# Optimization experiments

Measured on AMD Instinct MI355X. Metric: run time of the kernel, lower is better.

## Reference

```python
import jax, jax.numpy as jnp
import numpy as np

B, LQ, LKV, H, D, HS = 8, 32, 4096, 16, 64, 1024
ROPE_THETA = 10000.0
MAX_POS = 2080


def setup_inputs() -> dict:
    key = jax.random.key(0)
    ks = jax.random.split(key, 7)
    scale = 0.02
    return {
        "hidden_states": jax.random.normal(ks[0], (B, LQ, HS), dtype=jnp.float32),
        "encoder_hidden_states": jax.random.normal(ks[1], (B, LKV, HS), dtype=jnp.float32),
        "position_ids_q": jax.random.randint(ks[2], (B, LQ), 0, MAX_POS, dtype=jnp.int64),
        "Wq": jax.random.normal(ks[3], (HS, HS), dtype=jnp.float32) * scale,
        "Wk": jax.random.normal(ks[4], (HS, HS), dtype=jnp.float32) * scale,
        "Wv": jax.random.normal(ks[5], (HS, HS), dtype=jnp.float32) * scale,
        "Wo": jax.random.normal(ks[6], (HS, HS), dtype=jnp.float32) * scale,
    }


def _rotate_half(x):
    x1, x2 = jnp.split(x, 2, axis=-1)
    return jnp.concatenate([-x2, x1], axis=-1)


def _rope_cos_sin(position_ids):
    # LLaMA-style rotary embedding: inv_freq over even dims, emb = [freqs, freqs]
    inv_freq = 1.0 / (ROPE_THETA ** (jnp.arange(0, D, 2, dtype=jnp.float32) / D))
    freqs = position_ids.astype(jnp.float32)[..., None] * inv_freq  # [B, LQ, D/2]
    emb = jnp.concatenate([freqs, freqs], axis=-1)                  # [B, LQ, D]
    # broadcast over heads: [B, 1, LQ, D]
    return jnp.cos(emb)[:, None], jnp.sin(emb)[:, None]


def reference(hidden_states, encoder_hidden_states, position_ids_q, Wq, Wk, Wv, Wo):
    bsz, q_len, _ = hidden_states.shape
    kv_len = encoder_hidden_states.shape[1]
    # projections (weights stored [in, out])
    q = hidden_states @ Wq                       # [B, LQ, HS]
    k = encoder_hidden_states @ Wk               # [B, LKV, HS]
    v = encoder_hidden_states @ Wv               # [B, LKV, HS]
    # split heads -> [B, H, L, D]
    q = q.reshape(bsz, q_len, H, D).transpose(0, 2, 1, 3)
    k = k.reshape(bsz, kv_len, H, D).transpose(0, 2, 1, 3)
    v = v.reshape(bsz, kv_len, H, D).transpose(0, 2, 1, 3)
    # RoPE applied to QUERY ONLY (per original module)
    cos, sin = _rope_cos_sin(position_ids_q)
    q = q * cos + _rotate_half(q) * sin
    # scaled dot-product cross attention
    scores = jnp.einsum("bhqd,bhkd->bhqk", q, k) / jnp.sqrt(jnp.asarray(D, q.dtype))
    attn = jax.nn.softmax(scores, axis=-1)
    out = jnp.einsum("bhqk,bhkd->bhqd", attn, v)  # [B, H, LQ, D]
    out = out.transpose(0, 2, 1, 3).reshape(bsz, q_len, HS)
    return out @ Wo
```

## Files before the change

### kernel.cpp

```cpp
#include <hip/hip_runtime.h>


typedef float  f32x4  __attribute__((ext_vector_type(4)));
typedef __bf16 bf16x8 __attribute__((ext_vector_type(8)));

__device__ __forceinline__ ushort f2b(float x) {
  union { float f; unsigned u; } v; v.f = x;
  unsigned r = (v.u + 0x7fffu + ((v.u >> 16) & 1u)) >> 16;
  return (ushort)r;
}
__device__ __forceinline__ float b2f(ushort h) {
  union { unsigned u; float f; } v; v.u = ((unsigned)h) << 16; return v.f;
}
__device__ __forceinline__ void unpack2(unsigned v, float& lo, float& hi) {
  union { unsigned u; float f; } a, b;
  a.u = v << 16; b.u = v & 0xffff0000u;
  lo = a.f; hi = b.f;
}
__device__ __forceinline__ unsigned packb(float a, float b) {
  return (unsigned)f2b(a) | ((unsigned)f2b(b) << 16);
}
__device__ __forceinline__ int swz(int r) { return (r & 3) ^ ((r >> 2) & 3); }

__device__ __forceinline__ void gload16(const void* g, void* l) {
  __builtin_amdgcn_global_load_lds(
      (const __attribute__((address_space(1))) void*)g,
      (__attribute__((address_space(3))) void*)l, 16, 0, 0);
}

__global__ __launch_bounds__(256) void pack_x(
    const float* __restrict__ X, ushort* __restrict__ Xp1, ushort* __restrict__ Xp2) {
  const int z = blockIdx.z, jb = blockIdx.y, cb = blockIdx.x;
  const int t = threadIdx.x;
  __shared__ ushort sT[128 * 72];

#pragma unroll
  for (int rep = 0; rep < 2; ++rep) {
    const int j  = rep * 64 + (t >> 2);
    const int c0 = (t & 3) << 4;
    const float4* src = (const float4*)(X + ((size_t)z * 4096 + jb * 128 + j) * 1024 + cb * 64 + c0);
#pragma unroll
    for (int q = 0; q < 4; ++q) {
      const float4 v = src[q];
      ushort4 w; w.x = f2b(v.x); w.y = f2b(v.y); w.z = f2b(v.z); w.w = f2b(v.w);
      *(ushort4*)&sT[j * 72 + c0 + q * 4] = w;
    }
  }
  __syncthreads();

  ushort* o1 = Xp1 + ((size_t)(z * 32 + jb) * 32 + cb * 2) * 4096;
#pragma unroll
  for (int q = 0; q < 4; ++q) {
    const int kih = q >> 1;
    const int r   = ((q & 1) << 6) + (t >> 2);
    const int p   = t & 3;
    const int lc  = p ^ swz(r);
    const uint4 v = *(const uint4*)&sT[r * 72 + kih * 32 + lc * 8];
    *(uint4*)&o1[(size_t)kih * 4096 + ((size_t)(q & 1) << 11) + (size_t)t * 8] = v;
  }

  ushort* o2 = Xp2 + (((size_t)(z * 8 + (cb >> 1)) * 128 + jb * 4) * 4096) + ((size_t)(cb & 1) << 11);
#pragma unroll
  for (int q = 0; q < 4; ++q) {
    const int cl = t >> 2;
    const int p2 = t & 3;
    const int lj = p2 ^ swz(cl);
    union { ushort u[8]; uint4 v; } pk;
#pragma unroll
    for (int jj = 0; jj < 8; ++jj) pk.u[jj] = sT[(q * 32 + lj * 8 + jj) * 72 + cl];
    *(uint4*)&o2[(size_t)q * 4096 + (size_t)t * 8] = pk.v;
  }
}

__global__ __launch_bounds__(256) void pack_w(
    const float* __restrict__ Wq, const float* __restrict__ Wk,
    const float* __restrict__ Wv, const float* __restrict__ Wo,
    ushort* __restrict__ WqT, ushort* __restrict__ Wkb,
    ushort* __restrict__ WvT, ushort* __restrict__ WoT) {
  const int wsel = blockIdx.z;
  const float* src = (wsel == 0) ? Wq : (wsel == 1) ? Wk : (wsel == 2) ? Wv : Wo;
  const int row0 = blockIdx.y << 6, col0 = blockIdx.x << 6;
  const int t = threadIdx.x;
  __shared__ ushort sT[64 * 72];
  const int r = t >> 2, c0 = (t & 3) << 4;

  union { ushort u[16]; uint4 v[2]; } pk;
  const float4* s4 = (const float4*)(src + (size_t)(row0 + r) * 1024 + col0 + c0);
#pragma unroll
  for (int q = 0; q < 4; ++q) {
    const float4 v = s4[q];
    pk.u[q*4+0] = f2b(v.x); pk.u[q*4+1] = f2b(v.y);
    pk.u[q*4+2] = f2b(v.z); pk.u[q*4+3] = f2b(v.w);
  }
  if (wsel == 1) {
    ushort* dst = Wkb + (size_t)(row0 + r) * 1024 + col0 + c0;
    *(uint4*)dst = pk.v[0];
    *(uint4*)(dst + 8) = pk.v[1];
  } else {
#pragma unroll
    for (int q = 0; q < 16; ++q) sT[r * 72 + c0 + q] = pk.u[q];
    __syncthreads();
    ushort* dst = (wsel == 0) ? WqT : (wsel == 2) ? WvT : WoT;
    union { ushort u[16]; uint4 v[2]; } o;
#pragma unroll
    for (int q = 0; q < 16; ++q) o.u[q] = sT[(c0 + q) * 72 + r];
    ushort* d = dst + (size_t)(col0 + r) * 1024 + row0 + c0;
    *(uint4*)d = o.v[0];
    *(uint4*)(d + 8) = o.v[1];
  }
}

__global__ __launch_bounds__(256) void qrope_gemm(
    const float* __restrict__ hs, const ushort* __restrict__ WqT,
    float* __restrict__ qP) {
  __shared__ alignas(16) ushort sA[128 * 40];
  __shared__ alignas(16) ushort sB[128 * 40];
  const int nt = blockIdx.x, mt = blockIdx.y, ks = blockIdx.z;
  const int m0 = mt << 7, n0 = nt << 7, kb = ks << 8;
  const int t = threadIdx.x;
  const int wave = t >> 6, lane = t & 63;
  const int wm = wave >> 1, wn = wave & 1;
  const int fr = lane & 15, fq = lane >> 4;
  const int r = t >> 1, sg = (t & 1) << 4;

  f32x4 acc[4][4];
#pragma unroll
  for (int a = 0; a < 4; ++a)
#pragma unroll
    for (int c = 0; c < 4; ++c) acc[a][c] = (f32x4){0.f, 0.f, 0.f, 0.f};

  for (int it = 0; it < 8; ++it) {
    const int k0 = kb + (it << 5);
    {
      const float4* s4 = (const float4*)(hs + (size_t)(m0 + r) * 1024 + k0 + sg);
      union { ushort u[16]; uint4 v[2]; } pk;
#pragma unroll
      for (int q = 0; q < 4; ++q) {
        const float4 v = s4[q];
        pk.u[q*4+0] = f2b(v.x); pk.u[q*4+1] = f2b(v.y);
        pk.u[q*4+2] = f2b(v.z); pk.u[q*4+3] = f2b(v.w);
      }
      *(uint4*)&sA[r * 40 + sg]     = pk.v[0];
      *(uint4*)&sA[r * 40 + sg + 8] = pk.v[1];
    }
    {
      const uint4* s4 = (const uint4*)(WqT + (size_t)(n0 + r) * 1024 + k0 + sg);
      *(uint4*)&sB[r * 40 + sg]     = s4[0];
      *(uint4*)&sB[r * 40 + sg + 8] = s4[1];
    }
    __syncthreads();
    bf16x8 aF[4], bF[4];
#pragma unroll
    for (int u = 0; u < 4; ++u) {
      aF[u] = *(const bf16x8*)&sA[((wm << 6) + (u << 4) + fr) * 40 + (fq << 3)];
      bF[u] = *(const bf16x8*)&sB[((wn << 6) + (u << 4) + fr) * 40 + (fq << 3)];
    }
#pragma unroll
    for (int mi = 0; mi < 4; ++mi)
#pragma unroll
      for (int ni = 0; ni < 4; ++ni)
        acc[mi][ni] = __builtin_amdgcn_mfma_f32_16x16x32_bf16(
            aF[mi], bF[ni], acc[mi][ni], 0, 0, 0);
    __syncthreads();
  }
  float* dst = qP + (size_t)ks * 262144;
#pragma unroll
  for (int mi = 0; mi < 4; ++mi)
#pragma unroll
    for (int ni = 0; ni < 4; ++ni)
#pragma unroll
      for (int rr = 0; rr < 4; ++rr) {
        const int row = m0 + (wm << 6) + (mi << 4) + (fq << 2) + rr;
        const int col = n0 + (wn << 6) + (ni << 4) + fr;
        dst[(size_t)row * 1024 + col] = acc[mi][ni][rr];
      }
}

__global__ __launch_bounds__(256) void rope_apply(
    const float* __restrict__ qP, const int* __restrict__ pos,
    ushort* __restrict__ qr) {
  const int idx = blockIdx.x * 256 + threadIdx.x;
  const int m = idx >> 6;
  const int u = idx & 63;
  const int h = u >> 2;
  const int c8 = (u & 3) << 3;
  const int colx = h * 64 + c8;
  const int coly = colx + 32;

  float x[8], y[8];
#pragma unroll
  for (int j = 0; j < 8; ++j) { x[j] = 0.f; y[j] = 0.f; }
#pragma unroll
  for (int p = 0; p < 4; ++p) {
    const float* base = qP + (size_t)p * 262144 + (size_t)m * 1024;
    const float4 a0 = *(const float4*)(base + colx);
    const float4 a1 = *(const float4*)(base + colx + 4);
    const float4 b0 = *(const float4*)(base + coly);
    const float4 b1 = *(const float4*)(base + coly + 4);
    x[0]+=a0.x; x[1]+=a0.y; x[2]+=a0.z; x[3]+=a0.w;
    x[4]+=a1.x; x[5]+=a1.y; x[6]+=a1.z; x[7]+=a1.w;
    y[0]+=b0.x; y[1]+=b0.y; y[2]+=b0.z; y[3]+=b0.w;
    y[4]+=b1.x; y[5]+=b1.y; y[6]+=b1.z; y[7]+=b1.w;
  }

  unsigned oddor = 0;
  for (int j = 1; j < 256; j += 2) oddor |= (unsigned)pos[j];
  const int p = (oddor == 0) ? pos[2 * m] : pos[m];
  const float pf = (float)p;

  union { ushort u16[8]; uint4 v; } ox, oy;
#pragma unroll
  for (int j = 0; j < 8; ++j) {
    const int f = c8 + j;
    const float inv = powf(10000.0f, -(float)f * (1.0f / 32.0f));
    float sn, cs; sincosf(pf * inv, &sn, &cs);
    ox.u16[j] = f2b((x[j] * cs - y[j] * sn) * 0.125f);
    oy.u16[j] = f2b((y[j] * cs + x[j] * sn) * 0.125f);
  }
  *(uint4*)(qr + (size_t)m * 1024 + colx) = ox.v;
  *(uint4*)(qr + (size_t)m * 1024 + coly) = oy.v;
}

__global__ __launch_bounds__(256) void qk_gemm(
    const ushort* __restrict__ qr, const ushort* __restrict__ Wkb,
    ushort* __restrict__ qk) {
  __shared__ alignas(16) ushort sA[32 * 72];
  __shared__ alignas(16) ushort sB[256 * 72];
  const int nc = blockIdx.x, h = blockIdx.y, b = blockIdx.z;
  const int t = threadIdx.x;
  {
    const int i = t >> 3, seg = (t & 7) << 3;
    *(uint4*)&sA[i * 72 + seg] =
        *(const uint4*)(qr + (size_t)(b * 32 + i) * 1024 + h * 64 + seg);
  }
#pragma unroll
  for (int p = 0; p < 8; ++p) {
    const int rr = (t >> 3) + p * 32, seg = (t & 7) << 3;
    *(uint4*)&sB[rr * 72 + seg] =
        *(const uint4*)(Wkb + (size_t)(nc * 256 + rr) * 1024 + h * 64 + seg);
  }
  __syncthreads();

  const int wave = t >> 6, lane = t & 63;
  const int fr = lane & 15, fq = lane >> 4;
  f32x4 acc[2][4];
#pragma unroll
  for (int a = 0; a < 2; ++a)
#pragma unroll
    for (int c = 0; c < 4; ++c) acc[a][c] = (f32x4){0.f, 0.f, 0.f, 0.f};

#pragma unroll
  for (int ki = 0; ki < 2; ++ki) {
    bf16x8 aF[2], bF[4];
#pragma unroll
    for (int mi = 0; mi < 2; ++mi)
      aF[mi] = *(const bf16x8*)&sA[((mi << 4) + fr) * 72 + (ki << 5) + (fq << 3)];
#pragma unroll
    for (int ni = 0; ni < 4; ++ni)
      bF[ni] = *(const bf16x8*)&sB[((wave << 6) + (ni << 4) + fr) * 72 + (ki << 5) + (fq << 3)];
#pragma unroll
    for (int mi = 0; mi < 2; ++mi)
#pragma unroll
      for (int ni = 0; ni < 4; ++ni)
        acc[mi][ni] = __builtin_amdgcn_mfma_f32_16x16x32_bf16(
            aF[mi], bF[ni], acc[mi][ni], 0, 0, 0);
  }
#pragma unroll
  for (int mi = 0; mi < 2; ++mi)
#pragma unroll
    for (int ni = 0; ni < 4; ++ni)
#pragma unroll
      for (int rr = 0; rr < 4; ++rr) {
        const int row = h * 32 + (mi << 4) + (fq << 2) + rr;
        const int col = nc * 256 + (wave << 6) + (ni << 4) + fr;
        qk[((size_t)b * 512 + row) * 1024 + col] = f2b(acc[mi][ni][rr]);
      }
}

__global__ __launch_bounds__(256) void gemm1(
    const ushort* __restrict__ qk, const ushort* __restrict__ Xp1,
    ushort* __restrict__ Sc, float2* __restrict__ pstat) {
  __shared__ alignas(16) ushort sA[4096];
  __shared__ alignas(16) ushort sB[4096];
  __shared__ float sMx[256], sSm[256];
  const int z = blockIdx.x, nty = blockIdx.y, mt = blockIdx.z;
  const int tid = threadIdx.x;
  const int wave = tid >> 6, lane = tid & 63;
  const int wm = wave >> 1, wn = wave & 1;
  const int fr = lane & 15, fq = lane >> 4;
  const int sfr = swz(fr);
  const int srow = lane >> 2;
  const int lc   = (lane & 3) ^ swz(srow);

  const ushort* Ab = qk + ((size_t)z * 512 + mt * 128) * 1024;
  const ushort* Bb = Xp1 + ((size_t)(z * 32 + nty) * 32) * 4096;

  f32x4 acc[4][4];
#pragma unroll
  for (int a = 0; a < 4; ++a)
#pragma unroll
    for (int c = 0; c < 4; ++c) acc[a][c] = (f32x4){0.f, 0.f, 0.f, 0.f};

  for (int it = 0; it < 32; ++it) {
    const int k0 = it << 5;
    const ushort* Bc = Bb + (size_t)it * 4096 + wave * 1024;
#pragma unroll
    for (int seg = 0; seg < 2; ++seg) {
      gload16(Bc + seg * 512 + lane * 8, &sB[wave * 1024 + seg * 512]);
      const int row = wave * 32 + seg * 16 + srow;
      gload16(Ab + (size_t)row * 1024 + k0 + lc * 8, &sA[wave * 1024 + seg * 512]);
    }
    __syncthreads();
    bf16x8 aF[4], bF[4];
#pragma unroll
    for (int u = 0; u < 4; ++u) {
      aF[u] = *(const bf16x8*)&sA[((wm << 6) + (u << 4) + fr) * 32 + ((fq ^ sfr) << 3)];
      bF[u] = *(const bf16x8*)&sB[((wn << 6) + (u << 4) + fr) * 32 + ((fq ^ sfr) << 3)];
    }
#pragma unroll
    for (int mi = 0; mi < 4; ++mi)
#pragma unroll
      for (int nt = 0; nt < 4; ++nt)
        acc[mi][nt] = __builtin_amdgcn_mfma_f32_16x16x32_bf16(
            aF[mi], bF[nt], acc[mi][nt], 0, 0, 0);
    __syncthreads();
  }

  ushort* ScB = Sc + (size_t)(z * 4 + mt) * 524288;
#pragma unroll
  for (int mi = 0; mi < 4; ++mi)
#pragma unroll
    for (int nt = 0; nt < 4; ++nt)
#pragma unroll
      for (int r = 0; r < 4; ++r) {
        const int row = (wm << 6) + (mi << 4) + (fq << 2) + r;
        const int col = (wn << 6) + (nt << 4) + fr;
        const int ki  = (nty << 2) + (col >> 5);
        const int p   = ((col >> 3) & 3) ^ r ^ fq;
        const ushort hb = f2b(acc[mi][nt][r]);
        ScB[(size_t)ki * 4096 + row * 32 + p * 8 + (fr & 7)] = hb;
        acc[mi][nt][r] = b2f(hb);
      }

#pragma unroll
  for (int mi = 0; mi < 4; ++mi)
#pragma unroll
    for (int r = 0; r < 4; ++r) {
      float m4 = fmaxf(fmaxf(acc[mi][0][r], acc[mi][1][r]),
                       fmaxf(acc[mi][2][r], acc[mi][3][r]));
#pragma unroll
      for (int o = 1; o < 16; o <<= 1) m4 = fmaxf(m4, __shfl_xor(m4, o));
      float s4 = __expf(acc[mi][0][r] - m4) + __expf(acc[mi][1][r] - m4) +
                 __expf(acc[mi][2][r] - m4) + __expf(acc[mi][3][r] - m4);
#pragma unroll
      for (int o = 1; o < 16; o <<= 1) s4 += __shfl_xor(s4, o);
      if (fr == 0) {
        const int row = (wm << 6) + (mi << 4) + (fq << 2) + r;
        sMx[row * 2 + wn] = m4;
        sSm[row * 2 + wn] = s4;
      }
    }
  __syncthreads();
  if (tid < 128) {
    const float m0 = sMx[tid * 2], m1 = sMx[tid * 2 + 1];
    const float M = fmaxf(m0, m1);
    const float S = sSm[tid * 2] * __expf(m0 - M) + sSm[tid * 2 + 1] * __expf(m1 - M);
    pstat[((size_t)(z * 512 + mt * 128 + tid)) * 32 + nty] = make_float2(M, S);
  }
}

__global__ __launch_bounds__(256) void combine_stats(
    const float2* __restrict__ pstat, float2* __restrict__ stats2) {
  const int g = blockIdx.x * 256 + threadIdx.x;
  const float2* p = pstat + (size_t)g * 32;
  float M = -1e30f;
#pragma unroll
  for (int i = 0; i < 32; ++i) M = fmaxf(M, p[i].x);
  float S = 0.f;
#pragma unroll
  for (int i = 0; i < 32; ++i) S += p[i].y * __expf(p[i].x - M);
  stats2[g] = make_float2(M, 1.0f / S);
}

__global__ __launch_bounds__(256) void softmax_apply(
    ushort* __restrict__ Sc, const float2* __restrict__ stats2) {
  const size_t idx = (size_t)blockIdx.x * 256 + threadIdx.x;
  const int row = (int)((idx >> 16) * 128 + ((idx >> 2) & 127));
  const float2 st = stats2[row];
  uint4 v = *(uint4*)(Sc + idx * 8);
  float x0, x1, x2, x3, x4, x5, x6, x7;
  unpack2(v.x, x0, x1); unpack2(v.y, x2, x3);
  unpack2(v.z, x4, x5); unpack2(v.w, x6, x7);
  v.x = packb(__expf(x0 - st.x) * st.y, __expf(x1 - st.x) * st.y);
  v.y = packb(__expf(x2 - st.x) * st.y, __expf(x3 - st.x) * st.y);
  v.z = packb(__expf(x4 - st.x) * st.y, __expf(x5 - st.x) * st.y);
  v.w = packb(__expf(x6 - st.x) * st.y, __expf(x7 - st.x) * st.y);
  *(uint4*)(Sc + idx * 8) = v;
}

__global__ __launch_bounds__(256) void gemm2(
    const ushort* __restrict__ Sc, const ushort* __restrict__ Xp2,
    float* __restrict__ P) {
  __shared__ alignas(16) ushort sA[4096];
  __shared__ alignas(16) ushort sB[4096];
  const int z = blockIdx.x, nty = blockIdx.y;
  const int mt = blockIdx.z & 3, ks = blockIdx.z >> 2;
  const int tid = threadIdx.x;
  const int wave = tid >> 6, lane = tid & 63;
  const int wm = wave >> 1, wn = wave & 1;
  const int fr = lane & 15, fq = lane >> 4;
  const int sfr = swz(fr);

  const ushort* Ab = Sc + (size_t)(z * 4 + mt) * 524288 + (size_t)(ks * 32) * 4096;
  const ushort* Bb = Xp2 + ((size_t)(z * 8 + nty) * 128 + ks * 32) * 4096;

  f32x4 acc[4][4];
#pragma unroll
  for (int a = 0; a < 4; ++a)
#pragma unroll
    for (int c = 0; c < 4; ++c) acc[a][c] = (f32x4){0.f, 0.f, 0.f, 0.f};

  for (int it = 0; it < 32; ++it) {
    const ushort* Ac = Ab + (size_t)it * 4096 + wave * 1024;
    const ushort* Bc = Bb + (size_t)it * 4096 + wave * 1024;
#pragma unroll
    for (int seg = 0; seg < 2; ++seg) {
      gload16(Bc + seg * 512 + lane * 8, &sB[wave * 1024 + seg * 512]);
      gload16(Ac + seg * 512 + lane * 8, &sA[wave * 1024 + seg * 512]);
    }
    __syncthreads();
    bf16x8 aF[4], bF[4];
#pragma unroll
    for (int u = 0; u < 4; ++u) {
      aF[u] = *(const bf16x8*)&sA[((wm << 6) + (u << 4) + fr) * 32 + ((fq ^ sfr) << 3)];
      bF[u] = *(const bf16x8*)&sB[((wn << 6) + (u << 4) + fr) * 32 + ((fq ^ sfr) << 3)];
    }
#pragma unroll
    for (int mi = 0; mi < 4; ++mi)
#pragma unroll
      for (int nt = 0; nt < 4; ++nt)
        acc[mi][nt] = __builtin_amdgcn_mfma_f32_16x16x32_bf16(
            aF[mi], bF[nt], acc[mi][nt], 0, 0, 0);
    __syncthreads();
  }

  float* Pb = P + (((size_t)(ks * 8 + z) * 512) + mt * 128) * 1024 + nty * 128;
#pragma unroll
  for (int mi = 0; mi < 4; ++mi)
#pragma unroll
    for (int nt = 0; nt < 4; ++nt)
#pragma unroll
      for (int r = 0; r < 4; ++r) {
        const int row = (wm << 6) + (mi << 4) + (fq << 2) + r;
        const int col = (wn << 6) + (nt << 4) + fr;
        Pb[(size_t)row * 1024 + col] = acc[mi][nt][r];
      }
}

__global__ __launch_bounds__(256) void reduce4_bf16(
    const float* __restrict__ src, ushort* __restrict__ dst, long partStride) {
  const size_t i8 = ((size_t)blockIdx.x * 256 + threadIdx.x) * 8;
  float s[8];
#pragma unroll
  for (int j = 0; j < 8; ++j) s[j] = 0.f;
#pragma unroll
  for (int p = 0; p < 4; ++p) {
    const float4 a = *(const float4*)(src + (size_t)p * partStride + i8);
    const float4 b = *(const float4*)(src + (size_t)p * partStride + i8 + 4);
    s[0] += a.x; s[1] += a.y; s[2] += a.z; s[3] += a.w;
    s[4] += b.x; s[5] += b.y; s[6] += b.z; s[7] += b.w;
  }
  union { ushort u[8]; uint4 v; } o;
#pragma unroll
  for (int j = 0; j < 8; ++j) o.u[j] = f2b(s[j]);
  *(uint4*)(dst + i8) = o.v;
}

__global__ __launch_bounds__(256) void ctxwv_gemm(
    const ushort* __restrict__ ctx, const ushort* __restrict__ WvT,
    float* __restrict__ P2) {
  __shared__ alignas(16) ushort sA[32 * 264];
  __shared__ alignas(16) ushort sB[64 * 264];
  const int ks = blockIdx.x, h = blockIdx.y, b = blockIdx.z;
  const int kb = ks << 8;
  const int t = threadIdx.x;
#pragma unroll
  for (int p = 0; p < 4; ++p) {
    const int i = t >> 3, seg = ((t & 7) + p * 8) << 3;
    *(uint4*)&sA[i * 264 + seg] =
        *(const uint4*)(ctx + ((size_t)b * 512 + h * 32 + i) * 1024 + kb + seg);
  }
#pragma unroll
  for (int p = 0; p < 8; ++p) {
    const int rr = (t >> 3) + (p & 1) * 32;
    const int seg = ((t & 7) + (p >> 1) * 8) << 3;
    *(uint4*)&sB[rr * 264 + seg] =
        *(const uint4*)(WvT + (size_t)(h * 64 + rr) * 1024 + kb + seg);
  }
  __syncthreads();

  const int wave = t >> 6, lane = t & 63;
  const int fr = lane & 15, fq = lane >> 4;
  f32x4 acc[2];
  acc[0] = (f32x4){0.f, 0.f, 0.f, 0.f};
  acc[1] = (f32x4){0.f, 0.f, 0.f, 0.f};

#pragma unroll
  for (int ki = 0; ki < 8; ++ki) {
    bf16x8 bFr = *(const bf16x8*)&sB[((wave << 4) + fr) * 264 + (ki << 5) + (fq << 3)];
#pragma unroll
    for (int mi = 0; mi < 2; ++mi) {
      bf16x8 aF = *(const bf16x8*)&sA[((mi << 4) + fr) * 264 + (ki << 5) + (fq << 3)];
      acc[mi] = __builtin_amdgcn_mfma_f32_16x16x32_bf16(aF, bFr, acc[mi], 0, 0, 0);
    }
  }
  float* dst = P2 + (size_t)ks * 262144;
#pragma unroll
  for (int mi = 0; mi < 2; ++mi)
#pragma unroll
    for (int rr = 0; rr < 4; ++rr) {
      const int row = b * 32 + (mi << 4) + (fq << 2) + rr;
      const int col = h * 64 + (wave << 4) + fr;
      dst[(size_t)row * 1024 + col] = acc[mi][rr];
    }
}

__global__ __launch_bounds__(256) void out_gemm(
    const ushort* __restrict__ tmp2, const ushort* __restrict__ WoT,
    float* __restrict__ O4) {
  __shared__ alignas(16) ushort sA[128 * 40];
  __shared__ alignas(16) ushort sB[128 * 40];
  const int nt = blockIdx.x, mt = blockIdx.y, ks = blockIdx.z;
  const int m0 = mt << 7, n0 = nt << 7, kb = ks << 8;
  const int t = threadIdx.x;
  const int wave = t >> 6, lane = t & 63;
  const int wm = wave >> 1, wn = wave & 1;
  const int fr = lane & 15, fq = lane >> 4;
  const int r = t >> 1, sg = (t & 1) << 4;

  f32x4 acc[4][4];
#pragma unroll
  for (int a = 0; a < 4; ++a)
#pragma unroll
    for (int c = 0; c < 4; ++c) acc[a][c] = (f32x4){0.f, 0.f, 0.f, 0.f};

  for (int it = 0; it < 8; ++it) {
    const int k0 = kb + (it << 5);
    {
      const uint4* s4 = (const uint4*)(tmp2 + (size_t)(m0 + r) * 1024 + k0 + sg);
      *(uint4*)&sA[r * 40 + sg]     = s4[0];
      *(uint4*)&sA[r * 40 + sg + 8] = s4[1];
    }
    {
      const uint4* s4 = (const uint4*)(WoT + (size_t)(n0 + r) * 1024 + k0 + sg);
      *(uint4*)&sB[r * 40 + sg]     = s4[0];
      *(uint4*)&sB[r * 40 + sg + 8] = s4[1];
    }
    __syncthreads();
    bf16x8 aF[4], bF[4];
#pragma unroll
    for (int u = 0; u < 4; ++u) {
      aF[u] = *(const bf16x8*)&sA[((wm << 6) + (u << 4) + fr) * 40 + (fq << 3)];
      bF[u] = *(const bf16x8*)&sB[((wn << 6) + (u << 4) + fr) * 40 + (fq << 3)];
    }
#pragma unroll
    for (int mi = 0; mi < 4; ++mi)
#pragma unroll
      for (int ni = 0; ni < 4; ++ni)
        acc[mi][ni] = __builtin_amdgcn_mfma_f32_16x16x32_bf16(
            aF[mi], bF[ni], acc[mi][ni], 0, 0, 0);
    __syncthreads();
  }
  float* dst = O4 + (size_t)ks * 262144;
#pragma unroll
  for (int mi = 0; mi < 4; ++mi)
#pragma unroll
    for (int ni = 0; ni < 4; ++ni)
#pragma unroll
      for (int rr = 0; rr < 4; ++rr) {
        const int row = m0 + (wm << 6) + (mi << 4) + (fq << 2) + rr;
        const int col = n0 + (wn << 6) + (ni << 4) + fr;
        dst[(size_t)row * 1024 + col] = acc[mi][ni][rr];
      }
}

__global__ __launch_bounds__(256) void sum_out4(
    const float* __restrict__ O4, float* __restrict__ out) {
  const size_t i4 = ((size_t)blockIdx.x * 256 + threadIdx.x) * 4;
  float4 acc = *(const float4*)(O4 + i4);
#pragma unroll
  for (int p = 1; p < 4; ++p) {
    const float4 v = *(const float4*)(O4 + (size_t)p * 262144 + i4);
    acc.x += v.x; acc.y += v.y; acc.z += v.z; acc.w += v.w;
  }
  *(float4*)(out + i4) = acc;
}

extern "C" void kernel_launch(void* const* d_in, const int* in_sizes, int n_in,
                              void* d_out, int out_size, void* d_ws, size_t ws_size,
                              hipStream_t stream) {
  const float* hs  = (const float*)d_in[0];
  const float* enc = (const float*)d_in[1];
  const int*   pos = (const int*)d_in[2];
  const float* Wq  = (const float*)d_in[3];
  const float* Wk  = (const float*)d_in[4];
  const float* Wv  = (const float*)d_in[5];
  const float* Wo  = (const float*)d_in[6];
  float* out = (float*)d_out;

  char* w = (char*)d_ws;
  ushort* Xp1  = (ushort*)w;
  float*  P    = (float*)w;
  w += (size_t)67108864;
  ushort* Xp2  = (ushort*)w; w += (size_t)67108864;
  ushort* qk   = (ushort*)w;
  ushort* ctx  = (ushort*)w;
  w += (size_t)8388608;
  ushort* Sc   = (ushort*)w; w += (size_t)33554432;
  float2* pstat  = (float2*)w; w += (size_t)1048576;
  float2* stats2 = (float2*)w; w += (size_t)32768;
  ushort* qr   = (ushort*)w; w += (size_t)524288;
  ushort* tmp2 = (ushort*)w; w += (size_t)524288;
  float*  qP   = (float*)w;
  float*  P2   = (float*)w;
  float*  O4   = (float*)w;
  w += (size_t)4194304;

  ushort* WqT = (ushort*)w; w += (size_t)2097152;
  ushort* Wkb = (ushort*)w; w += (size_t)2097152;
  ushort* WvT = (ushort*)w; w += (size_t)2097152;
  ushort* WoT = (ushort*)w; w += (size_t)2097152;

  pack_x<<<dim3(16, 32, 8), 256, 0, stream>>>(enc, Xp1, Xp2);
  pack_w<<<dim3(16, 16, 4), 256, 0, stream>>>(Wq, Wk, Wv, Wo, WqT, Wkb, WvT, WoT);
  qrope_gemm<<<dim3(8, 2, 4), 256, 0, stream>>>(hs, WqT, qP);
  rope_apply<<<64, 256, 0, stream>>>(qP, pos, qr);
  qk_gemm<<<dim3(4, 16, 8), 256, 0, stream>>>(qr, Wkb, qk);
  gemm1<<<dim3(8, 32, 4), 256, 0, stream>>>(qk, Xp1, Sc, pstat);
  combine_stats<<<16, 256, 0, stream>>>(pstat, stats2);
  softmax_apply<<<8192, 256, 0, stream>>>(Sc, stats2);
  gemm2<<<dim3(8, 8, 16), 256, 0, stream>>>(Sc, Xp2, P);
  reduce4_bf16<<<2048, 256, 0, stream>>>(P, ctx, 4194304L);
  ctxwv_gemm<<<dim3(4, 16, 8), 256, 0, stream>>>(ctx, WvT, P2);
  reduce4_bf16<<<128, 256, 0, stream>>>(P2, tmp2, 262144L);
  out_gemm<<<dim3(8, 2, 4), 256, 0, stream>>>(tmp2, WoT, O4);
  sum_out4<<<256, 256, 0, stream>>>(O4, out);
}
```

Before: 469.0 us.

## Fuse rope, softmax and split-K reductions into adjacent GEMMs; widen K tiles

Folds rope_apply into the qk GEMM, softmax_apply into the P·V GEMM's A-tile load, and both reduce4 passes into the consumer GEMMs' A loads. This removes four kernel launches and several full round-trips through global memory, notably the read-modify-write of the large score buffer. It also doubles the K tile per iteration in gemm1 and gemm2 and halves gemm2's split-K count. In exchange the A loads do more arithmetic, the partial-sum reads are redone by every consumer block, and shared memory per block doubles, which may lower occupancy.

```diff
diff --git a/kernel.cpp b/kernel.cpp
--- a/kernel.cpp
+++ b/kernel.cpp
@@ -176,62 +176,30 @@
       }
 }
 
-__global__ __launch_bounds__(256) void rope_apply(
-    const float* __restrict__ qP, const int* __restrict__ pos,
-    ushort* __restrict__ qr) {
-  const int idx = blockIdx.x * 256 + threadIdx.x;
-  const int m = idx >> 6;
-  const int u = idx & 63;
-  const int h = u >> 2;
-  const int c8 = (u & 3) << 3;
-  const int colx = h * 64 + c8;
-  const int coly = colx + 32;
-
-  float x[8], y[8];
-#pragma unroll
-  for (int j = 0; j < 8; ++j) { x[j] = 0.f; y[j] = 0.f; }
-#pragma unroll
-  for (int p = 0; p < 4; ++p) {
-    const float* base = qP + (size_t)p * 262144 + (size_t)m * 1024;
-    const float4 a0 = *(const float4*)(base + colx);
-    const float4 a1 = *(const float4*)(base + colx + 4);
-    const float4 b0 = *(const float4*)(base + coly);
-    const float4 b1 = *(const float4*)(base + coly + 4);
-    x[0]+=a0.x; x[1]+=a0.y; x[2]+=a0.z; x[3]+=a0.w;
-    x[4]+=a1.x; x[5]+=a1.y; x[6]+=a1.z; x[7]+=a1.w;
-    y[0]+=b0.x; y[1]+=b0.y; y[2]+=b0.z; y[3]+=b0.w;
-    y[4]+=b1.x; y[5]+=b1.y; y[6]+=b1.z; y[7]+=b1.w;
-  }
-
-  unsigned oddor = 0;
-  for (int j = 1; j < 256; j += 2) oddor |= (unsigned)pos[j];
-  const int p = (oddor == 0) ? pos[2 * m] : pos[m];
-  const float pf = (float)p;
-
-  union { ushort u16[8]; uint4 v; } ox, oy;
-#pragma unroll
-  for (int j = 0; j < 8; ++j) {
-    const int f = c8 + j;
-    const float inv = powf(10000.0f, -(float)f * (1.0f / 32.0f));
-    float sn, cs; sincosf(pf * inv, &sn, &cs);
-    ox.u16[j] = f2b((x[j] * cs - y[j] * sn) * 0.125f);
-    oy.u16[j] = f2b((y[j] * cs + x[j] * sn) * 0.125f);
-  }
-  *(uint4*)(qr + (size_t)m * 1024 + colx) = ox.v;
-  *(uint4*)(qr + (size_t)m * 1024 + coly) = oy.v;
-}
-
-__global__ __launch_bounds__(256) void qk_gemm(
-    const ushort* __restrict__ qr, const ushort* __restrict__ Wkb,
-    ushort* __restrict__ qk) {
+__global__ __launch_bounds__(256) void qk_rope_gemm(
+    const float* __restrict__ qP, const ushort* __restrict__ Wkb,
+    const int* __restrict__ pos, ushort* __restrict__ qk) {
+  __shared__ float s_qf[32 * 68];
   __shared__ alignas(16) ushort sA[32 * 72];
   __shared__ alignas(16) ushort sB[256 * 72];
   const int nc = blockIdx.x, h = blockIdx.y, b = blockIdx.z;
   const int t = threadIdx.x;
+  const int i = t >> 3, d0 = (t & 7) << 3;
+
   {
-    const int i = t >> 3, seg = (t & 7) << 3;
-    *(uint4*)&sA[i * 72 + seg] =
-        *(const uint4*)(qr + (size_t)(b * 32 + i) * 1024 + h * 64 + seg);
+    float s[8];
+#pragma unroll
+    for (int j = 0; j < 8; ++j) s[j] = 0.f;
+#pragma unroll
+    for (int p = 0; p < 4; ++p) {
+      const float* base = qP + (size_t)p * 262144 + (size_t)(b * 32 + i) * 1024 + h * 64 + d0;
+      const float4 a0 = *(const float4*)base;
+      const float4 a1 = *(const float4*)(base + 4);
+      s[0]+=a0.x; s[1]+=a0.y; s[2]+=a0.z; s[3]+=a0.w;
+      s[4]+=a1.x; s[5]+=a1.y; s[6]+=a1.z; s[7]+=a1.w;
+    }
+#pragma unroll
+    for (int j = 0; j < 8; ++j) s_qf[i * 68 + d0 + j] = s[j];
   }
 #pragma unroll
   for (int p = 0; p < 8; ++p) {
@@ -241,6 +209,28 @@
   }
   __syncthreads();
 
+  {
+    unsigned oddor = 0;
+    for (int j = 1; j < 256; j += 2) oddor |= (unsigned)pos[j];
+    const int m = b * 32 + i;
+    const int p = (oddor == 0) ? pos[2 * m] : pos[m];
+    const float pf = (float)p;
+    union { ushort u16[8]; uint4 v; } o;
+#pragma unroll
+    for (int j = 0; j < 8; ++j) {
+      const int d = d0 + j;
+      const int f = d & 31;
+      const float inv = powf(10000.0f, -(float)f * (1.0f / 32.0f));
+      float sn, cs; sincosf(pf * inv, &sn, &cs);
+      const float x  = s_qf[i * 68 + d];
+      const float xp = s_qf[i * 68 + (d ^ 32)];
+      const float v  = (d < 32) ? (x * cs - xp * sn) : (x * cs + xp * sn);
+      o.u16[j] = f2b(v * 0.125f);
+    }
+    *(uint4*)&sA[i * 72 + d0] = o.v;
+  }
+  __syncthreads();
+
   const int wave = t >> 6, lane = t & 63;
   const int fr = lane & 15, fq = lane >> 4;
   f32x4 acc[2][4];
@@ -280,8 +270,8 @@
 __global__ __launch_bounds__(256) void gemm1(
     const ushort* __restrict__ qk, const ushort* __restrict__ Xp1,
     ushort* __restrict__ Sc, float2* __restrict__ pstat) {
-  __shared__ alignas(16) ushort sA[4096];
-  __shared__ alignas(16) ushort sB[4096];
+  __shared__ alignas(16) ushort sA[8192];
+  __shared__ alignas(16) ushort sB[8192];
   __shared__ float sMx[256], sSm[256];
   const int z = blockIdx.x, nty = blockIdx.y, mt = blockIdx.z;
   const int tid = threadIdx.x;
@@ -289,40 +279,49 @@
   const int wm = wave >> 1, wn = wave & 1;
   const int fr = lane & 15, fq = lane >> 4;
   const int sfr = swz(fr);
-  const int srow = lane >> 2;
-  const int lc   = (lane & 3) ^ swz(srow);
 
   const ushort* Ab = qk + ((size_t)z * 512 + mt * 128) * 1024;
   const ushort* Bb = Xp1 + ((size_t)(z * 32 + nty) * 32) * 4096;
 
+  int arow[4], aoff[4];
+#pragma unroll
+  for (int j = 0; j < 4; ++j) {
+    const int rowA = ((wave & 1) << 6) + (j << 4) + (lane >> 2);
+    arow[j] = rowA;
+    aoff[j] = ((wave >> 1) << 5) + (((lane & 3) ^ swz(rowA)) << 3);
+  }
+
   f32x4 acc[4][4];
 #pragma unroll
   for (int a = 0; a < 4; ++a)
 #pragma unroll
     for (int c = 0; c < 4; ++c) acc[a][c] = (f32x4){0.f, 0.f, 0.f, 0.f};
 
-  for (int it = 0; it < 32; ++it) {
-    const int k0 = it << 5;
-    const ushort* Bc = Bb + (size_t)it * 4096 + wave * 1024;
-#pragma unroll
-    for (int seg = 0; seg < 2; ++seg) {
-      gload16(Bc + seg * 512 + lane * 8, &sB[wave * 1024 + seg * 512]);
-      const int row = wave * 32 + seg * 16 + srow;
-      gload16(Ab + (size_t)row * 1024 + k0 + lc * 8, &sA[wave * 1024 + seg * 512]);
-    }
-    __syncthreads();
-    bf16x8 aF[4], bF[4];
-#pragma unroll
-    for (int u = 0; u < 4; ++u) {
-      aF[u] = *(const bf16x8*)&sA[((wm << 6) + (u << 4) + fr) * 32 + ((fq ^ sfr) << 3)];
-      bF[u] = *(const bf16x8*)&sB[((wn << 6) + (u << 4) + fr) * 32 + ((fq ^ sfr) << 3)];
-    }
-#pragma unroll
-    for (int mi = 0; mi < 4; ++mi)
-#pragma unroll
-      for (int nt = 0; nt < 4; ++nt)
-        acc[mi][nt] = __builtin_amdgcn_mfma_f32_16x16x32_bf16(
-            aF[mi], bF[nt], acc[mi][nt], 0, 0, 0);
+  for (int it = 0; it < 16; ++it) {
+    const int k0 = it << 6;
+#pragma unroll
+    for (int j = 0; j < 4; ++j) {
+      gload16(Bb + (size_t)it * 8192 + wave * 2048 + j * 512 + lane * 8,
+              &sB[wave * 2048 + j * 512]);
+      gload16(Ab + (size_t)arow[j] * 1024 + k0 + aoff[j],
+              &sA[wave * 2048 + j * 512]);
+    }
+    __syncthreads();
+#pragma unroll
+    for (int kk = 0; kk < 2; ++kk) {
+      bf16x8 aF[4], bF[4];
+#pragma unroll
+      for (int u = 0; u < 4; ++u) {
+        aF[u] = *(const bf16x8*)&sA[kk * 4096 + ((wm << 6) + (u << 4) + fr) * 32 + ((fq ^ sfr) << 3)];
+        bF[u] = *(const bf16x8*)&sB[kk * 4096 + ((wn << 6) + (u << 4) + fr) * 32 + ((fq ^ sfr) << 3)];
+      }
+#pragma unroll
+      for (int mi = 0; mi < 4; ++mi)
+#pragma unroll
+        for (int ni = 0; ni < 4; ++ni)
+          acc[mi][ni] = __builtin_amdgcn_mfma_f32_16x16x32_bf16(
+              aF[mi], bF[ni], acc[mi][ni], 0, 0, 0);
+    }
     __syncthreads();
   }
 
@@ -330,16 +329,16 @@
 #pragma unroll
   for (int mi = 0; mi < 4; ++mi)
 #pragma unroll
-    for (int nt = 0; nt < 4; ++nt)
+    for (int ni = 0; ni < 4; ++ni)
 #pragma unroll
       for (int r = 0; r < 4; ++r) {
         const int row = (wm << 6) + (mi << 4) + (fq << 2) + r;
-        const int col = (wn << 6) + (nt << 4) + fr;
+        const int col = (wn << 6) + (ni << 4) + fr;
         const int ki  = (nty << 2) + (col >> 5);
         const int p   = ((col >> 3) & 3) ^ r ^ fq;
-        const ushort hb = f2b(acc[mi][nt][r]);
+        const ushort hb = f2b(acc[mi][ni][r]);
         ScB[(size_t)ki * 4096 + row * 32 + p * 8 + (fr & 7)] = hb;
-        acc[mi][nt][r] = b2f(hb);
+        acc[mi][ni][r] = b2f(hb);
       }
 
 #pragma unroll
@@ -382,37 +381,24 @@
   stats2[g] = make_float2(M, 1.0f / S);
 }
 
-__global__ __launch_bounds__(256) void softmax_apply(
-    ushort* __restrict__ Sc, const float2* __restrict__ stats2) {
-  const size_t idx = (size_t)blockIdx.x * 256 + threadIdx.x;
-  const int row = (int)((idx >> 16) * 128 + ((idx >> 2) & 127));
-  const float2 st = stats2[row];
-  uint4 v = *(uint4*)(Sc + idx * 8);
-  float x0, x1, x2, x3, x4, x5, x6, x7;
-  unpack2(v.x, x0, x1); unpack2(v.y, x2, x3);
-  unpack2(v.z, x4, x5); unpack2(v.w, x6, x7);
-  v.x = packb(__expf(x0 - st.x) * st.y, __expf(x1 - st.x) * st.y);
-  v.y = packb(__expf(x2 - st.x) * st.y, __expf(x3 - st.x) * st.y);
-  v.z = packb(__expf(x4 - st.x) * st.y, __expf(x5 - st.x) * st.y);
-  v.w = packb(__expf(x6 - st.x) * st.y, __expf(x7 - st.x) * st.y);
-  *(uint4*)(Sc + idx * 8) = v;
-}
-
-__global__ __launch_bounds__(256) void gemm2(
+__global__ __launch_bounds__(256) void gemm2f(
     const ushort* __restrict__ Sc, const ushort* __restrict__ Xp2,
-    float* __restrict__ P) {
-  __shared__ alignas(16) ushort sA[4096];
-  __shared__ alignas(16) ushort sB[4096];
+    const float2* __restrict__ stats2, float* __restrict__ P) {
+  __shared__ alignas(16) ushort sA[8192];
+  __shared__ alignas(16) ushort sB[8192];
   const int z = blockIdx.x, nty = blockIdx.y;
-  const int mt = blockIdx.z & 3, ks = blockIdx.z >> 2;
+  const int mt = blockIdx.z & 3, s = blockIdx.z >> 2;
   const int tid = threadIdx.x;
   const int wave = tid >> 6, lane = tid & 63;
   const int wm = wave >> 1, wn = wave & 1;
   const int fr = lane & 15, fq = lane >> 4;
   const int sfr = swz(fr);
 
-  const ushort* Ab = Sc + (size_t)(z * 4 + mt) * 524288 + (size_t)(ks * 32) * 4096;
-  const ushort* Bb = Xp2 + ((size_t)(z * 8 + nty) * 128 + ks * 32) * 4096;
+  const ushort* Ab = Sc + (size_t)(z * 4 + mt) * 524288 + (size_t)s * 262144;
+  const ushort* Bb = Xp2 + ((size_t)(z * 8 + nty) * 128 + s * 64) * 4096;
+
+  const float2 st0 = stats2[z * 512 + mt * 128 + (tid >> 2)];
+  const float2 st1 = stats2[z * 512 + mt * 128 + 64 + (tid >> 2)];
 
   f32x4 acc[4][4];
 #pragma unroll
@@ -421,63 +407,59 @@
     for (int c = 0; c < 4; ++c) acc[a][c] = (f32x4){0.f, 0.f, 0.f, 0.f};
 
   for (int it = 0; it < 32; ++it) {
-    const ushort* Ac = Ab + (size_t)it * 4096 + wave * 1024;
-    const ushort* Bc = Bb + (size_t)it * 4096 + wave * 1024;
-#pragma unroll
-    for (int seg = 0; seg < 2; ++seg) {
-      gload16(Bc + seg * 512 + lane * 8, &sB[wave * 1024 + seg * 512]);
-      gload16(Ac + seg * 512 + lane * 8, &sA[wave * 1024 + seg * 512]);
-    }
-    __syncthreads();
-    bf16x8 aF[4], bF[4];
-#pragma unroll
-    for (int u = 0; u < 4; ++u) {
-      aF[u] = *(const bf16x8*)&sA[((wm << 6) + (u << 4) + fr) * 32 + ((fq ^ sfr) << 3)];
-      bF[u] = *(const bf16x8*)&sB[((wn << 6) + (u << 4) + fr) * 32 + ((fq ^ sfr) << 3)];
-    }
-#pragma unroll
-    for (int mi = 0; mi < 4; ++mi)
-#pragma unroll
-      for (int nt = 0; nt < 4; ++nt)
-        acc[mi][nt] = __builtin_amdgcn_mfma_f32_16x16x32_bf16(
-            aF[mi], bF[nt], acc[mi][nt], 0, 0, 0);
-    __syncthreads();
-  }
-
-  float* Pb = P + (((size_t)(ks * 8 + z) * 512) + mt * 128) * 1024 + nty * 128;
+#pragma unroll
+    for (int j = 0; j < 4; ++j)
+      gload16(Bb + (size_t)it * 8192 + wave * 2048 + j * 512 + lane * 8,
+              &sB[wave * 2048 + j * 512]);
+#pragma unroll
+    for (int j = 0; j < 4; ++j) {
+      const uint4 v = *(const uint4*)(Ab + (size_t)it * 8192 + j * 2048 + tid * 8);
+      const float M   = (j & 1) ? st1.x : st0.x;
+      const float inv = (j & 1) ? st1.y : st0.y;
+      float x0,x1,x2,x3,x4,x5,x6,x7;
+      unpack2(v.x, x0, x1); unpack2(v.y, x2, x3);
+      unpack2(v.z, x4, x5); unpack2(v.w, x6, x7);
+      uint4 o;
+      o.x = packb(__expf(x0 - M) * inv, __expf(x1 - M) * inv);
+      o.y = packb(__expf(x2 - M) * inv, __expf(x3 - M) * inv);
+      o.z = packb(__expf(x4 - M) * inv, __expf(x5 - M) * inv);
+      o.w = packb(__expf(x6 - M) * inv, __expf(x7 - M) * inv);
+      *(uint4*)&sA[j * 2048 + tid * 8] = o;
+    }
+    __syncthreads();
+#pragma unroll
+    for (int kk = 0; kk < 2; ++kk) {
+      bf16x8 aF[4], bF[4];
+#pragma unroll
+      for (int u = 0; u < 4; ++u) {
+        aF[u] = *(const bf16x8*)&sA[kk * 4096 + ((wm << 6) + (u << 4) + fr) * 32 + ((fq ^ sfr) << 3)];
+        bF[u] = *(const bf16x8*)&sB[kk * 4096 + ((wn << 6) + (u << 4) + fr) * 32 + ((fq ^ sfr) << 3)];
+      }
+#pragma unroll
+      for (int mi = 0; mi < 4; ++mi)
+#pragma unroll
+        for (int ni = 0; ni < 4; ++ni)
+          acc[mi][ni] = __builtin_amdgcn_mfma_f32_16x16x32_bf16(
+              aF[mi], bF[ni], acc[mi][ni], 0, 0, 0);
+    }
+    __syncthreads();
+  }
+
+  float* Pb = P + (((size_t)(s * 8 + z) * 512) + mt * 128) * 1024 + nty * 128;
 #pragma unroll
   for (int mi = 0; mi < 4; ++mi)
 #pragma unroll
-    for (int nt = 0; nt < 4; ++nt)
+    for (int ni = 0; ni < 4; ++ni)
 #pragma unroll
       for (int r = 0; r < 4; ++r) {
         const int row = (wm << 6) + (mi << 4) + (fq << 2) + r;
-        const int col = (wn << 6) + (nt << 4) + fr;
-        Pb[(size_t)row * 1024 + col] = acc[mi][nt][r];
-      }
-}
-
-__global__ __launch_bounds__(256) void reduce4_bf16(
-    const float* __restrict__ src, ushort* __restrict__ dst, long partStride) {
-  const size_t i8 = ((size_t)blockIdx.x * 256 + threadIdx.x) * 8;
-  float s[8];
-#pragma unroll
-  for (int j = 0; j < 8; ++j) s[j] = 0.f;
-#pragma unroll
-  for (int p = 0; p < 4; ++p) {
-    const float4 a = *(const float4*)(src + (size_t)p * partStride + i8);
-    const float4 b = *(const float4*)(src + (size_t)p * partStride + i8 + 4);
-    s[0] += a.x; s[1] += a.y; s[2] += a.z; s[3] += a.w;
-    s[4] += b.x; s[5] += b.y; s[6] += b.z; s[7] += b.w;
-  }
-  union { ushort u[8]; uint4 v; } o;
-#pragma unroll
-  for (int j = 0; j < 8; ++j) o.u[j] = f2b(s[j]);
-  *(uint4*)(dst + i8) = o.v;
+        const int col = (wn << 6) + (ni << 4) + fr;
+        Pb[(size_t)row * 1024 + col] = acc[mi][ni][r];
+      }
 }
 
 __global__ __launch_bounds__(256) void ctxwv_gemm(
-    const ushort* __restrict__ ctx, const ushort* __restrict__ WvT,
+    const float* __restrict__ P, const ushort* __restrict__ WvT,
     float* __restrict__ P2) {
   __shared__ alignas(16) ushort sA[32 * 264];
   __shared__ alignas(16) ushort sB[64 * 264];
@@ -485,10 +467,18 @@
   const int kb = ks << 8;
   const int t = threadIdx.x;
 #pragma unroll
-  for (int p = 0; p < 4; ++p) {
-    const int i = t >> 3, seg = ((t & 7) + p * 8) << 3;
-    *(uint4*)&sA[i * 264 + seg] =
-        *(const uint4*)(ctx + ((size_t)b * 512 + h * 32 + i) * 1024 + kb + seg);
+  for (int q = 0; q < 4; ++q) {
+    const int i = t >> 3, seg = ((t & 7) + q * 8) << 3;
+    const float* p0 = P + ((size_t)(0 * 8 + b) * 512 + h * 32 + i) * 1024 + kb + seg;
+    const float* p1 = P + ((size_t)(1 * 8 + b) * 512 + h * 32 + i) * 1024 + kb + seg;
+    const float4 a0 = *(const float4*)p0,       a1 = *(const float4*)(p0 + 4);
+    const float4 b0 = *(const float4*)p1,       b1 = *(const float4*)(p1 + 4);
+    uint4 o;
+    o.x = packb(a0.x + b0.x, a0.y + b0.y);
+    o.y = packb(a0.z + b0.z, a0.w + b0.w);
+    o.z = packb(a1.x + b1.x, a1.y + b1.y);
+    o.w = packb(a1.z + b1.z, a1.w + b1.w);
+    *(uint4*)&sA[i * 264 + seg] = o;
   }
 #pragma unroll
   for (int p = 0; p < 8; ++p) {
@@ -526,7 +516,7 @@
 }
 
 __global__ __launch_bounds__(256) void out_gemm(
-    const ushort* __restrict__ tmp2, const ushort* __restrict__ WoT,
+    const float* __restrict__ P2, const ushort* __restrict__ WoT,
     float* __restrict__ O4) {
   __shared__ alignas(16) ushort sA[128 * 40];
   __shared__ alignas(16) ushort sB[128 * 40];
@@ -547,9 +537,25 @@
   for (int it = 0; it < 8; ++it) {
     const int k0 = kb + (it << 5);
     {
-      const uint4* s4 = (const uint4*)(tmp2 + (size_t)(m0 + r) * 1024 + k0 + sg);
-      *(uint4*)&sA[r * 40 + sg]     = s4[0];
-      *(uint4*)&sA[r * 40 + sg + 8] = s4[1];
+      float s[16];
+#pragma unroll
+      for (int j = 0; j < 16; ++j) s[j] = 0.f;
+#pragma unroll
+      for (int p = 0; p < 4; ++p) {
+        const float* base = P2 + (size_t)p * 262144 + (size_t)(m0 + r) * 1024 + k0 + sg;
+#pragma unroll
+        for (int q = 0; q < 4; ++q) {
+          const float4 v = *(const float4*)(base + q * 4);
+          s[q*4+0] += v.x; s[q*4+1] += v.y; s[q*4+2] += v.z; s[q*4+3] += v.w;
+        }
+      }
+      uint4 o0, o1;
+      o0.x = packb(s[0], s[1]);   o0.y = packb(s[2], s[3]);
+      o0.z = packb(s[4], s[5]);   o0.w = packb(s[6], s[7]);
+      o1.x = packb(s[8], s[9]);   o1.y = packb(s[10], s[11]);
+      o1.z = packb(s[12], s[13]); o1.w = packb(s[14], s[15]);
+      *(uint4*)&sA[r * 40 + sg]     = o0;
+      *(uint4*)&sA[r * 40 + sg + 8] = o1;
     }
     {
       const uint4* s4 = (const uint4*)(WoT + (size_t)(n0 + r) * 1024 + k0 + sg);
@@ -612,20 +618,16 @@
   ushort* Xp1  = (ushort*)w;
   float*  P    = (float*)w;
   w += (size_t)67108864;
-  ushort* Xp2  = (ushort*)w; w += (size_t)67108864;
-  ushort* qk   = (ushort*)w;
-  ushort* ctx  = (ushort*)w;
-  w += (size_t)8388608;
+  ushort* Xp2  = (ushort*)w;
+  float*  P2   = (float*)w;
+  w += (size_t)67108864;
+  ushort* qk   = (ushort*)w; w += (size_t)8388608;
   ushort* Sc   = (ushort*)w; w += (size_t)33554432;
   float2* pstat  = (float2*)w; w += (size_t)1048576;
   float2* stats2 = (float2*)w; w += (size_t)32768;
-  ushort* qr   = (ushort*)w; w += (size_t)524288;
-  ushort* tmp2 = (ushort*)w; w += (size_t)524288;
   float*  qP   = (float*)w;
-  float*  P2   = (float*)w;
   float*  O4   = (float*)w;
   w += (size_t)4194304;
-
   ushort* WqT = (ushort*)w; w += (size_t)2097152;
   ushort* Wkb = (ushort*)w; w += (size_t)2097152;
   ushort* WvT = (ushort*)w; w += (size_t)2097152;
@@ -634,15 +636,11 @@
   pack_x<<<dim3(16, 32, 8), 256, 0, stream>>>(enc, Xp1, Xp2);
   pack_w<<<dim3(16, 16, 4), 256, 0, stream>>>(Wq, Wk, Wv, Wo, WqT, Wkb, WvT, WoT);
   qrope_gemm<<<dim3(8, 2, 4), 256, 0, stream>>>(hs, WqT, qP);
-  rope_apply<<<64, 256, 0, stream>>>(qP, pos, qr);
-  qk_gemm<<<dim3(4, 16, 8), 256, 0, stream>>>(qr, Wkb, qk);
+  qk_rope_gemm<<<dim3(4, 16, 8), 256, 0, stream>>>(qP, Wkb, pos, qk);
   gemm1<<<dim3(8, 32, 4), 256, 0, stream>>>(qk, Xp1, Sc, pstat);
   combine_stats<<<16, 256, 0, stream>>>(pstat, stats2);
-  softmax_apply<<<8192, 256, 0, stream>>>(Sc, stats2);
-  gemm2<<<dim3(8, 8, 16), 256, 0, stream>>>(Sc, Xp2, P);
-  reduce4_bf16<<<2048, 256, 0, stream>>>(P, ctx, 4194304L);
-  ctxwv_gemm<<<dim3(4, 16, 8), 256, 0, stream>>>(ctx, WvT, P2);
-  reduce4_bf16<<<128, 256, 0, stream>>>(P2, tmp2, 262144L);
-  out_gemm<<<dim3(8, 2, 4), 256, 0, stream>>>(tmp2, WoT, O4);
+  gemm2f<<<dim3(8, 8, 8), 256, 0, stream>>>(Sc, Xp2, stats2, P);
+  ctxwv_gemm<<<dim3(4, 16, 8), 256, 0, stream>>>(P, WvT, P2);
+  out_gemm<<<dim3(8, 2, 4), 256, 0, stream>>>(P2, WoT, O4);
   sum_out4<<<256, 256, 0, stream>>>(O4, out);
 }
```

Measured after the change: 442.1 us. -5.7%, faster.
